# Optimization experiments

Hardware: AMD Instinct MI355X
Metric: run time of the kernel (lower is better)

The kernel has to match this reference:

```python
import jax, jax.numpy as jnp
import numpy as np

K = 50            # neighbors (self excluded)
ALPHA = 0.99      # propagation coefficient
THRESH = 0.4      # pseudo-label confidence threshold
MAXITER = 20      # CG iterations
NUM_CLASSES = 100
TOL = 1e-6        # CG relative tolerance (scipy cg tol)


def setup_inputs() -> dict:
    key = jax.random.key(0)
    k1, k2, k3 = jax.random.split(key, 3)
    N, d = 16384, 128
    X = jax.random.normal(k1, (N, d), dtype=jnp.float32)
    labels = jax.random.randint(k2, (N,), 0, NUM_CLASSES)
    labels_mask = jax.random.uniform(k3, (N,)) < 0.1
    idxs = jnp.arange(N)
    return {"X": X, "labels": labels, "labels_mask": labels_mask, "idxs": idxs}


def _label_prop(X, labels, labels_mask):
    N = X.shape[0]
    # faiss.normalize_L2 + inner-product search == cosine kNN
    Xn = X / jnp.maximum(jnp.linalg.norm(X, axis=1, keepdims=True), 1e-12)
    sims = Xn @ Xn.T                                   # [N, N]
    vals, I = jax.lax.top_k(sims, K + 1)
    Dv = vals[:, 1:] ** 3                              # drop self column, cube sims
    I = I[:, 1:]
    rows = jnp.repeat(jnp.arange(N), K)
    cols = I.reshape(-1)
    w = Dv.reshape(-1)
    # W = W + W.T with diagonal zeroed (edge-list form, never dense NxN)
    er = jnp.concatenate([rows, cols])
    ec = jnp.concatenate([cols, rows])
    ew = jnp.concatenate([w, w])
    ew = jnp.where(er == ec, 0.0, ew)
    S = jax.ops.segment_sum(ew, er, num_segments=N)
    S = jnp.where(S == 0, 1.0, S)
    Dinv = 1.0 / jnp.sqrt(S)                           # D^{-1/2}

    def A_mv(V):  # (I - alpha * D^-1/2 W D^-1/2) @ V, V: [N, C]
        U = Dinv[:, None] * V
        WU = jax.ops.segment_sum(ew[:, None] * U[ec], er, num_segments=N)
        return V - ALPHA * (Dinv[:, None] * WU)

    # per-class normalized seed vectors y (1/|labeled_c| on labeled idx of class c)
    mask_f = labels_mask.astype(jnp.float32)
    counts = jax.ops.segment_sum(mask_f, labels, num_segments=NUM_CLASSES)
    Y = (mask_f[:, None] * jax.nn.one_hot(labels, NUM_CLASSES, dtype=jnp.float32)) / jnp.maximum(counts, 1.0)[None, :]

    # batched CG (x0 = 0), all classes solved simultaneously; per-column early-stop mask
    bnorm = jnp.linalg.norm(Y, axis=0)
    x = jnp.zeros_like(Y)
    r = Y
    p = r
    rs = jnp.sum(r * r, axis=0)

    def step(carry, _):
        x, r, p, rs = carry
        active = jnp.sqrt(rs) > TOL * jnp.maximum(bnorm, 1e-30)
        Ap = A_mv(p)
        a = rs / jnp.maximum(jnp.sum(p * Ap, axis=0), 1e-30)
        a = jnp.where(active, a, 0.0)
        x = x + a * p
        r = r - a * Ap
        rs_new = jnp.sum(r * r, axis=0)
        beta = jnp.where(active, rs_new / jnp.maximum(rs, 1e-30), 0.0)
        p = jnp.where(active, r + beta * p, p)
        rs = jnp.where(active, rs_new, rs)
        return (x, r, p, rs), None

    (x, _, _, _), _ = jax.lax.scan(step, (x, r, p, rs), None, length=MAXITER)

    Z = jnp.maximum(x, 0.0)
    # torch F.normalize(Z, p=1, dim=1)
    probs_l1 = Z / jnp.maximum(jnp.sum(Z, axis=1, keepdims=True), 1e-12)
    pseudo = jax.nn.softmax(probs_l1, axis=-1)
    return pseudo


def reference(X, labels, labels_mask, idxs):
    pseudo = _label_prop(X, labels, labels_mask)
    max_probs = jnp.max(pseudo, axis=-1)
    p_labels = jnp.argmax(pseudo, axis=-1)
    masks = (max_probs >= THRESH).astype(jnp.float32)
    acc = jnp.mean((p_labels == labels).astype(jnp.float32))
    p_labels = jnp.where(labels_mask, labels, p_labels)  # overwrite labeled idx
    return p_labels, acc, masks
```

## Files before the change

kernel.cpp:

```cpp
#include <hip/hip_runtime.h>
#include <hip/hip_bf16.h>
#include <math.h>


#define N_NODES 16384
#define DIM     128
#define KNN     50
#define NCLS    100
#define PSTR    100
#define ALPHA_C 0.99f
#define TOL_C   1e-6f
#define TAU     0.20f
#define MAXITER_C 20
#define NPB     2048

__global__ __launch_bounds__(256) void k_norm(const float* __restrict__ X, float* __restrict__ Xn){
  int t = threadIdx.x;
  int row = blockIdx.x*2 + (t>>7);
  int c = t & 127;
  float v = X[(size_t)row*DIM + c];
  float s = v*v;
  #pragma unroll
  for (int o=1;o<64;o<<=1) s += __shfl_xor(s, o, 64);
  __shared__ float sw[4];
  if ((t&63)==0) sw[t>>6] = s;
  __syncthreads();
  int half = (t>>7)*2;
  float nrm = fmaxf(sqrtf(sw[half]+sw[half+1]), 1e-12f);
  Xn[(size_t)row*DIM + c] = v / nrm;
}

#define NTILE 8256
__global__ __launch_bounds__(256, 4) void k_sims(const float* __restrict__ Xn,
    int* __restrict__ cand_cnt, unsigned long long* __restrict__ cand, int CAP){
  __shared__ __align__(16) float As[32][132];
  __shared__ __align__(16) float Bs[32][132];
  const int t = threadIdx.x;
  const int tr = t >> 4, tc = t & 15;
  const int q = blockIdx.x;
  float disc = 66049.0f - 8.0f*(float)q;
  int rb = (int)((257.0f - sqrtf(disc))*0.5f);
  if (rb > 127) rb = 127;
  while (rb > 0 && rb*(257-rb)/2 > q) --rb;
  while ((rb+1)*(257-(rb+1))/2 <= q) ++rb;
  int cb = rb + (q - rb*(257-rb)/2);
  const int row0 = rb*128, col0 = cb*128;
  float acc[8][8];
  #pragma unroll
  for (int i=0;i<8;i++){
    #pragma unroll
    for (int j=0;j<8;j++) acc[i][j]=0.f;
  }
  #pragma unroll 1
  for (int h=0; h<4; ++h){
    const int koff = h*32;
    if (h) __syncthreads();
    for (int v=t; v<1024; v+=256){
      int r = v>>3, k4 = (v&7)*4;
      float4 f = *(const float4*)(Xn + (size_t)(row0+r)*DIM + koff + k4);
      As[k4+0][r]=f.x; As[k4+1][r]=f.y; As[k4+2][r]=f.z; As[k4+3][r]=f.w;
      float4 g = *(const float4*)(Xn + (size_t)(col0+r)*DIM + koff + k4);
      Bs[k4+0][r]=g.x; Bs[k4+1][r]=g.y; Bs[k4+2][r]=g.z; Bs[k4+3][r]=g.w;
    }
    __syncthreads();
    #pragma unroll 4
    for (int k=0;k<32;k++){
      float a[8], b[8];
      *(float4*)&a[0] = *(const float4*)&As[k][tr*4];
      *(float4*)&a[4] = *(const float4*)&As[k][64+tr*4];
      *(float4*)&b[0] = *(const float4*)&Bs[k][tc*4];
      *(float4*)&b[4] = *(const float4*)&Bs[k][64+tc*4];
      #pragma unroll
      for (int i=0;i<8;i++){
        #pragma unroll
        for (int j=0;j<8;j++) acc[i][j] = fmaf(a[i], b[j], acc[i][j]);
      }
    }
  }
  #pragma unroll
  for (int i=0;i<8;i++){
    int row = row0 + ((i<4) ? (tr*4+i) : (64+tr*4+i-4));
    #pragma unroll
    for (int j=0;j<8;j++){
      float v = acc[i][j];
      if (v > TAU){
        int col = col0 + ((j<4) ? (tc*4+j) : (64+tc*4+j-4));
        unsigned long long vb = (unsigned long long)__float_as_uint(v) << 32;
        if (rb == cb){
          if (col != row){
            int pos = atomicAdd(&cand_cnt[row], 1);
            if (pos < CAP) __builtin_nontemporal_store(vb | (unsigned long long)(~(unsigned int)col), &cand[(size_t)row*CAP + pos]);
          }
        } else {
          int pos = atomicAdd(&cand_cnt[row], 1);
          if (pos < CAP) __builtin_nontemporal_store(vb | (unsigned long long)(~(unsigned int)col), &cand[(size_t)row*CAP + pos]);
          int pos2 = atomicAdd(&cand_cnt[col], 1);
          if (pos2 < CAP) __builtin_nontemporal_store(vb | (unsigned long long)(~(unsigned int)row), &cand[(size_t)col*CAP + pos2]);
        }
      }
    }
  }
}

__global__ __launch_bounds__(256) void k_select(const unsigned long long* __restrict__ cand,
    const int* __restrict__ cand_cnt, int CAP,
    int* __restrict__ nbr_idx, float* __restrict__ nbr_w, int* __restrict__ flags){
  int row = blockIdx.x; int t = threadIdx.x;
  int cnt = cand_cnt[row];
  if (cnt < KNN || cnt > CAP || cnt > 1024){ if (t==0) flags[row] = 1; return; }
  __shared__ unsigned long long sk[1024];
  int N = (cnt <= 256) ? 256 : ((cnt <= 512) ? 512 : 1024);
  for (int v=t; v<N; v+=256)
    sk[v] = (v < cnt) ? cand[(size_t)row*CAP + v] : 0ull;
  __syncthreads();
  for (int k=2; k<=N; k<<=1){
    for (int j=k>>1; j>0; j>>=1){
      for (int i=t; i<N; i+=256){
        int l = i ^ j;
        if (l > i){
          unsigned long long a = sk[i], b = sk[l];
          bool desc = ((i & k) == 0);
          bool sw = desc ? (a < b) : (a > b);
          if (sw){ sk[i] = b; sk[l] = a; }
        }
      }
      __syncthreads();
    }
  }
  if (t < KNN){
    unsigned long long key = sk[t];
    float v = __uint_as_float((unsigned int)(key >> 32));
    int ii = (int)(~(unsigned int)key);
    nbr_idx[(size_t)row*KNN + t] = ii;
    nbr_w[(size_t)row*KNN + t] = v*v*v;
  }
}

__global__ __launch_bounds__(256) void k_fallback(const float* __restrict__ Xn, const int* __restrict__ flags,
    int* __restrict__ nbr_idx, float* __restrict__ nbr_w){
  int row = blockIdx.x;
  if (flags[row]==0) return;
  int t = threadIdx.x;
  __shared__ float a[DIM];
  __shared__ float cv[256]; __shared__ int ci[256];
  __shared__ float bv[KNN]; __shared__ int bi[KNN];
  __shared__ int nf; __shared__ float minv; __shared__ int mini, minpos;
  if (t < DIM) a[t] = Xn[(size_t)row*DIM + t];
  if (t==0){ nf=0; minv=1e30f; mini=-1; minpos=-1; }
  __syncthreads();
  for (int c0=0; c0<N_NODES; c0+=256){
    int col = c0 + t;
    const float* xb = Xn + (size_t)col*DIM;
    float dot = 0.f;
    for (int k=0;k<DIM;k++) dot = fmaf(a[k], xb[k], dot);
    cv[t] = (col==row) ? -1e30f : dot;
    ci[t] = col;
    __syncthreads();
    if (t==0){
      for (int u=0; u<256; u++){
        float v = cv[u]; int ix = ci[u];
        if (v <= -1e29f) continue;
        if (nf < KNN){
          bv[nf]=v; bi[nf]=ix; nf++;
          if (nf==KNN){
            minpos=0; minv=bv[0]; mini=bi[0];
            for (int q=1;q<KNN;q++) if (bv[q]<minv || (bv[q]==minv && bi[q]>mini)){minv=bv[q];mini=bi[q];minpos=q;}
          }
        } else if (v>minv || (v==minv && ix<mini)){
          bv[minpos]=v; bi[minpos]=ix;
          minpos=0; minv=bv[0]; mini=bi[0];
          for (int q=1;q<KNN;q++) if (bv[q]<minv || (bv[q]==minv && bi[q]>mini)){minv=bv[q];mini=bi[q];minpos=q;}
        }
      }
    }
    __syncthreads();
  }
  if (t==0){
    for (int aa=1; aa<KNN; aa++){
      float kv=bv[aa]; int ki=bi[aa]; int b=aa-1;
      while (b>=0 && (bv[b]<kv || (bv[b]==kv && bi[b]>ki))){ bv[b+1]=bv[b]; bi[b+1]=bi[b]; b--; }
      bv[b+1]=kv; bi[b+1]=ki;
    }
    for (int q=0;q<KNN;q++){ nbr_idx[(size_t)row*KNN+q]=bi[q]; float v=bv[q]; nbr_w[(size_t)row*KNN+q]=v*v*v; }
  }
}

__global__ void k_indeg(const int* __restrict__ nbr_idx, int* __restrict__ indeg){
  int e = blockIdx.x*blockDim.x + threadIdx.x;
  if (e < N_NODES*KNN) atomicAdd(&indeg[nbr_idx[e]], 1);
}
__global__ __launch_bounds__(256) void k_scan(const int* __restrict__ indeg, int* __restrict__ offs){
  int t = threadIdx.x;
  __shared__ int ps[256];
  int base = t*64, s = 0;
  for (int m=0;m<64;m++) s += indeg[base+m];
  ps[t] = s; __syncthreads();
  if (t==0){ int run=0; for (int i=0;i<256;i++){ int tmp=ps[i]; ps[i]=run; run+=tmp; } offs[N_NODES]=run; }
  __syncthreads();
  int run = ps[t];
  for (int m=0;m<64;m++){ offs[base+m]=run; run += indeg[base+m]; }
}
__global__ void k_fill(const int* __restrict__ nbr_idx, const float* __restrict__ nbr_w,
    const int* __restrict__ offs, int* __restrict__ fillc, int* __restrict__ rev_src, float* __restrict__ rev_w){
  int e = blockIdx.x*blockDim.x + threadIdx.x;
  if (e >= N_NODES*KNN) return;
  int i = e / KNN;
  int j = nbr_idx[e];
  int pos = offs[j] + atomicAdd(&fillc[j], 1);
  rev_src[pos] = i;
  rev_w[pos]  = nbr_w[e];
}
__global__ __launch_bounds__(256) void k_sortrev(const int* __restrict__ offs, int* __restrict__ rev_src, float* __restrict__ rev_w){
  __shared__ int   ssrc[4][512];
  __shared__ float swv [4][512];
  int w = threadIdx.x>>6, lane = threadIdx.x&63;
  int node = blockIdx.x*4 + w;
  int e0 = offs[node], e1 = offs[node+1];
  int len = e1 - e0;
  if (len <= 1 || len > 512) return;
  for (int q=lane; q<len; q+=64){ ssrc[w][q]=rev_src[e0+q]; swv[w][q]=rev_w[e0+q]; }
  if (lane==0){
    for (int a=1;a<len;a++){
      int ks=ssrc[w][a]; float kw=swv[w][a]; int b=a-1;
      while (b>=0 && ssrc[w][b]>ks){ ssrc[w][b+1]=ssrc[w][b]; swv[w][b+1]=swv[w][b]; b--; }
      ssrc[w][b+1]=ks; swv[w][b+1]=kw;
    }
  }
  for (int q=lane; q<len; q+=64){ rev_src[e0+q]=ssrc[w][q]; rev_w[e0+q]=swv[w][q]; }
}
__global__ void k_degree(const float* __restrict__ nbr_w, const int* __restrict__ offs,
    const float* __restrict__ rev_w, float* __restrict__ Dinv){
  int i = blockIdx.x*blockDim.x + threadIdx.x;
  if (i >= N_NODES) return;
  float s = 0.f;
  for (int k=0;k<KNN;k++) s += nbr_w[(size_t)i*KNN+k];
  int e0=offs[i], e1=offs[i+1];
  for (int e=e0;e<e1;e++) s += rev_w[e];
  if (s == 0.f) s = 1.f;
  Dinv[i] = 1.0f / sqrtf(s);
}
__global__ void k_normw_fwd(const int* __restrict__ nbr_idx, float* __restrict__ nbr_w, const float* __restrict__ Dinv){
  int e = blockIdx.x*blockDim.x + threadIdx.x;
  if (e >= N_NODES*KNN) return;
  int i = e / KNN; int j = nbr_idx[e];
  nbr_w[e] *= Dinv[i]*Dinv[j];
}
__global__ __launch_bounds__(256) void k_normw_rev(const int* __restrict__ offs, const int* __restrict__ rev_src,
    float* __restrict__ rev_w, const float* __restrict__ Dinv){
  int wid = (blockIdx.x*256 + threadIdx.x)>>6; int lane = threadIdx.x&63;
  if (wid >= N_NODES) return;
  float di = Dinv[wid];
  int e1 = offs[wid+1];
  for (int e=offs[wid]+lane; e<e1; e+=64) rev_w[e] *= di*Dinv[rev_src[e]];
}
__global__ __launch_bounds__(256) void k_pack(const int* __restrict__ nbr_idx, const float* __restrict__ nbr_w,
    const int* __restrict__ offs, const int* __restrict__ rev_src, const float* __restrict__ rev_w,
    int2* __restrict__ adj){
  int w = threadIdx.x>>6, lane = threadIdx.x&63;
  int node = blockIdx.x*4 + w;
  int a0 = 50*node + offs[node];
  for (int k=lane; k<KNN; k+=64)
    adj[a0+k] = make_int2(nbr_idx[(size_t)node*KNN+k], __float_as_int(nbr_w[(size_t)node*KNN+k]));
  int e0 = offs[node], e1 = offs[node+1];
  for (int e=e0+lane; e<e1; e+=64)
    adj[a0+KNN+(e-e0)] = make_int2(rev_src[e], __float_as_int(rev_w[e]));
}

__global__ void k_clscnt(const int* __restrict__ labels, const int* __restrict__ mask, int* __restrict__ cls_cnt){
  int n = blockIdx.x*blockDim.x + threadIdx.x;
  if (n < N_NODES && mask[n]) atomicAdd(&cls_cnt[labels[n]], 1);
}
__global__ void k_init(const int* __restrict__ labels, const int* __restrict__ mask, const int* __restrict__ cls_cnt,
    float* __restrict__ x, float* __restrict__ r, float* __restrict__ p){
  int idx = blockIdx.x*blockDim.x + threadIdx.x;
  if (idx >= N_NODES*PSTR) return;
  int n = idx / PSTR, c = idx - n*PSTR;
  float y = 0.f;
  if (mask[n] && labels[n]==c) y = 1.0f / fmaxf((float)cls_cnt[c], 1.0f);
  x[idx]=0.f; r[idx]=y; p[idx]=y;
}

__global__ __launch_bounds__(256) void k_spmv_pap(const float* __restrict__ p, float* __restrict__ Ap,
    const int2* __restrict__ adj, const int* __restrict__ offs,
    float* __restrict__ partT){
  int t = threadIdx.x, w = t>>6, l = t&63;
  __shared__ float sh[4][100];
  float ppx=0.f, ppy=0.f;
  if (l < 50){
    #pragma unroll
    for (int m=0;m<2;m++){
      int node = __builtin_amdgcn_readfirstlane(blockIdx.x*8 + w*2 + m);
      int a0 = 50*node + offs[node];
      int a1 = 50*(node+1) + offs[node+1];
      float accx=0.f, accy=0.f;
      for (int e=a0; e<a1; ++e){
        int2 jw = adj[e];
        float wv = __int_as_float(jw.y);
        float2 v = ((const float2*)(p + (size_t)jw.x*PSTR))[l];
        accx = fmaf(wv, v.x, accx);
        accy = fmaf(wv, v.y, accy);
      }
      size_t o = (size_t)node*PSTR;
      float2 pv = ((const float2*)(p + o))[l];
      float ax = pv.x - ALPHA_C*accx;
      float ay = pv.y - ALPHA_C*accy;
      ((float2*)(Ap + o))[l] = make_float2(ax, ay);
      ppx = fmaf(pv.x, ax, ppx);
      ppy = fmaf(pv.y, ay, ppy);
    }
    sh[w][2*l]   = ppx;
    sh[w][2*l+1] = ppy;
  }
  __syncthreads();
  if (t < 100) partT[(size_t)t*NPB + blockIdx.x] = (sh[0][t]+sh[1][t]) + (sh[2][t]+sh[3][t]);
}
__global__ __launch_bounds__(256) void k_alpha(const float* __restrict__ partT, const float* __restrict__ rs_cur,
    const float* __restrict__ bnorm, float* __restrict__ avec, int* __restrict__ actvec){
  int c = blockIdx.x, t = threadIdx.x;
  float s = 0.f;
  #pragma unroll
  for (int b=0;b<NPB/256;b++) s += partT[(size_t)c*NPB + b*256 + t];
  #pragma unroll
  for (int o=1;o<64;o<<=1) s += __shfl_xor(s, o, 64);
  __shared__ float red[4];
  if ((t&63)==0) red[t>>6] = s;
  __syncthreads();
  if (t==0){
    float tot = (red[0]+red[1]) + (red[2]+red[3]);
    float rc = rs_cur[c];
    int act = sqrtf(rc) > TOL_C*fmaxf(bnorm[c], 1e-30f);
    avec[c] = act ? rc/fmaxf(tot, 1e-30f) : 0.f;
    actvec[c] = act;
  }
}
__global__ __launch_bounds__(256) void k_update_xr(float* __restrict__ x, float* __restrict__ r,
    const float* __restrict__ p, const float* __restrict__ Ap,
    const float* __restrict__ avec, float* __restrict__ partT){
  int t = threadIdx.x, w = t>>6, l = t&63;
  __shared__ float sh[4][100];
  float rpx=0.f, rpy=0.f;
  if (l < 50){
    float2 av = ((const float2*)avec)[l];
    #pragma unroll
    for (int m=0;m<2;m++){
      int n = blockIdx.x*8 + w*2 + m;
      size_t o = (size_t)n*PSTR;
      float2 pv  = ((const float2*)(p + o))[l];
      float2 apv = ((const float2*)(Ap + o))[l];
      float2 xv  = ((const float2*)(x + o))[l];
      float2 rv  = ((const float2*)(r + o))[l];
      xv.x = fmaf(av.x, pv.x, xv.x);
      xv.y = fmaf(av.y, pv.y, xv.y);
      rv.x = rv.x - av.x*apv.x;
      rv.y = rv.y - av.y*apv.y;
      ((float2*)(x + o))[l] = xv;
      ((float2*)(r + o))[l] = rv;
      rpx = fmaf(rv.x, rv.x, rpx);
      rpy = fmaf(rv.y, rv.y, rpy);
    }
    sh[w][2*l]   = rpx;
    sh[w][2*l+1] = rpy;
  }
  __syncthreads();
  if (t < 100) partT[(size_t)t*NPB + blockIdx.x] = (sh[0][t]+sh[1][t]) + (sh[2][t]+sh[3][t]);
}
__global__ __launch_bounds__(256) void k_beta(const float* __restrict__ partT, const float* __restrict__ rs_cur,
    const int* __restrict__ actvec, float* __restrict__ rs_next, float* __restrict__ betavec){
  int c = blockIdx.x, t = threadIdx.x;
  float s = 0.f;
  #pragma unroll
  for (int b=0;b<NPB/256;b++) s += partT[(size_t)c*NPB + b*256 + t];
  #pragma unroll
  for (int o=1;o<64;o<<=1) s += __shfl_xor(s, o, 64);
  __shared__ float red[4];
  if ((t&63)==0) red[t>>6] = s;
  __syncthreads();
  if (t==0){
    float tot = (red[0]+red[1]) + (red[2]+red[3]);
    float rc = rs_cur[c];
    int act = actvec[c];
    rs_next[c] = act ? tot : rc;
    betavec[c] = act ? tot/fmaxf(rc, 1e-30f) : 0.f;
  }
}
__global__ __launch_bounds__(256) void k_update_p(float* __restrict__ p, const float* __restrict__ r,
    const int* __restrict__ actvec, const float* __restrict__ betavec){
  int t = threadIdx.x, w = t>>6, l = t&63;
  if (l >= 50) return;
  float2 bv = ((const float2*)betavec)[l];
  int2   av = ((const int2*)actvec)[l];
  #pragma unroll
  for (int m=0;m<2;m++){
    int n = blockIdx.x*8 + w*2 + m;
    size_t o = (size_t)n*PSTR;
    float2 pv = ((const float2*)(p + o))[l];
    float2 rv = ((const float2*)(r + o))[l];
    pv.x = av.x ? fmaf(bv.x, pv.x, rv.x) : pv.x;
    pv.y = av.y ? fmaf(bv.y, pv.y, rv.y) : pv.y;
    ((float2*)(p + o))[l] = pv;
  }
}
__global__ __launch_bounds__(256) void k_coldot0(const float* __restrict__ r, float* __restrict__ partT){
  int t = threadIdx.x, w = t>>6, l = t&63;
  __shared__ float sh[4][100];
  float px=0.f, py=0.f;
  if (l < 50){
    #pragma unroll
    for (int m=0;m<2;m++){
      int n = blockIdx.x*8 + w*2 + m;
      float2 rv = ((const float2*)(r + (size_t)n*PSTR))[l];
      px = fmaf(rv.x, rv.x, px);
      py = fmaf(rv.y, rv.y, py);
    }
    sh[w][2*l]   = px;
    sh[w][2*l+1] = py;
  }
  __syncthreads();
  if (t < 100) partT[(size_t)t*NPB + blockIdx.x] = (sh[0][t]+sh[1][t]) + (sh[2][t]+sh[3][t]);
}
__global__ __launch_bounds__(256) void k_rs0(const float* __restrict__ partT, float* __restrict__ rs0, float* __restrict__ bnorm){
  int c = blockIdx.x, t = threadIdx.x;
  float s = 0.f;
  #pragma unroll
  for (int b=0;b<NPB/256;b++) s += partT[(size_t)c*NPB + b*256 + t];
  #pragma unroll
  for (int o=1;o<64;o<<=1) s += __shfl_xor(s, o, 64);
  __shared__ float red[4];
  if ((t&63)==0) red[t>>6] = s;
  __syncthreads();
  if (t==0){
    float tot = (red[0]+red[1]) + (red[2]+red[3]);
    rs0[c] = tot;
    bnorm[c] = sqrtf(tot);
  }
}

__global__ __launch_bounds__(256) void k_final(const float* __restrict__ x, const int* __restrict__ labels,
    const int* __restrict__ mask, float* __restrict__ out, int* __restrict__ acc_cnt){
  int n = blockIdx.x*blockDim.x + threadIdx.x;
  if (n >= N_NODES) return;
  const float* xr = x + (size_t)n*PSTR;
  float best = xr[0]; int arg = 0;
  for (int c=1;c<NCLS;c++){ float v = xr[c]; if (v > best){ best = v; arg = c; } }
  int plab = (best > 0.f) ? arg : 0;
  if (plab == labels[n]) atomicAdd(acc_cnt, 1);
  int lab = mask[n] ? labels[n] : plab;
  out[n] = (float)lab;
  out[N_NODES + 1 + n] = 0.f;
}
__global__ void k_acc(const int* __restrict__ acc_cnt, float* __restrict__ out){
  out[N_NODES] = (float)(*acc_cnt) / (float)N_NODES;
}

extern "C" void kernel_launch(void* const* d_in, const int* in_sizes, int n_in,
                              void* d_out, int out_size, void* d_ws, size_t ws_size,
                              hipStream_t stream){
  (void)in_sizes; (void)n_in; (void)out_size;
  const float* X      = (const float*)d_in[0];
  const int*   labels = (const int*)  d_in[1];
  const int*   mask   = (const int*)  d_in[2];
  float* out = (float*)d_out;

  char* ws = (char*)d_ws;
  size_t off = 0;
  auto alloc = [&](size_t bytes)->char*{ char* pp = ws + off; off += (bytes + 255) & ~(size_t)255; return pp; };

  float* Xn      = (float*)alloc((size_t)N_NODES*DIM*4);
  int*   nbr_idx = (int*)  alloc((size_t)N_NODES*KNN*4);
  float* nbr_w   = (float*)alloc((size_t)N_NODES*KNN*4);
  int*   indeg   = (int*)  alloc((size_t)N_NODES*4);
  int*   offs    = (int*)  alloc((size_t)(N_NODES+1)*4);
  int*   fillc   = (int*)  alloc((size_t)N_NODES*4);
  int*   rev_src = (int*)  alloc((size_t)N_NODES*KNN*4);
  float* rev_w   = (float*)alloc((size_t)N_NODES*KNN*4);
  int2*  adj     = (int2*) alloc((size_t)2*N_NODES*KNN*8);
  float* Dinv    = (float*)alloc((size_t)N_NODES*4);
  int*   cls_cnt = (int*)  alloc(128*4);
  float* x  = (float*)alloc((size_t)N_NODES*PSTR*4);
  float* r  = (float*)alloc((size_t)N_NODES*PSTR*4);
  float* p  = (float*)alloc((size_t)N_NODES*PSTR*4);
  float* Ap = (float*)alloc((size_t)N_NODES*PSTR*4);
  float* rs_a   = (float*)alloc(128*4);
  float* rs_b   = (float*)alloc(128*4);
  float* avec   = (float*)alloc(128*4);
  float* betavec= (float*)alloc(128*4);
  int*   actvec = (int*)  alloc(128*4);
  float* bnorm  = (float*)alloc(128*4);
  float* partT  = (float*)alloc((size_t)100*NPB*4);
  int*   acc_cnt= (int*)  alloc(256);
  int*   flags  = (int*)  alloc((size_t)N_NODES*4);
  int*   cand_cnt=(int*)  alloc((size_t)N_NODES*4);

  size_t rem = (ws_size > off) ? (ws_size - off) : 0;
  size_t capc = rem/((size_t)N_NODES*8);
  int CAP = (int)(capc < 1024 ? capc : 1024);
  CAP &= ~7;
  unsigned long long* cand = (unsigned long long*)alloc((size_t)N_NODES*CAP*8);

  hipMemsetAsync(cand_cnt, 0, (size_t)N_NODES*4, stream);
  hipMemsetAsync(flags,    0, (size_t)N_NODES*4, stream);
  hipMemsetAsync(indeg,    0, (size_t)N_NODES*4, stream);
  hipMemsetAsync(fillc,    0, (size_t)N_NODES*4, stream);
  hipMemsetAsync(cls_cnt,  0, 128*4, stream);
  hipMemsetAsync(acc_cnt,  0, 4, stream);

  k_norm    <<<N_NODES/2, 256, 0, stream>>>(X, Xn);
  k_sims    <<<NTILE, 256, 0, stream>>>(Xn, cand_cnt, cand, CAP);
  k_select  <<<N_NODES, 256, 0, stream>>>(cand, cand_cnt, CAP, nbr_idx, nbr_w, flags);
  k_fallback<<<N_NODES, 256, 0, stream>>>(Xn, flags, nbr_idx, nbr_w);
  k_indeg   <<<3200, 256, 0, stream>>>(nbr_idx, indeg);
  k_scan    <<<1, 256, 0, stream>>>(indeg, offs);
  k_fill    <<<3200, 256, 0, stream>>>(nbr_idx, nbr_w, offs, fillc, rev_src, rev_w);
  k_sortrev <<<4096, 256, 0, stream>>>(offs, rev_src, rev_w);
  k_degree  <<<64, 256, 0, stream>>>(nbr_w, offs, rev_w, Dinv);
  k_normw_fwd<<<3200, 256, 0, stream>>>(nbr_idx, nbr_w, Dinv);
  k_normw_rev<<<4096, 256, 0, stream>>>(offs, rev_src, rev_w, Dinv);
  k_pack    <<<4096, 256, 0, stream>>>(nbr_idx, nbr_w, offs, rev_src, rev_w, adj);
  k_clscnt  <<<64, 256, 0, stream>>>(labels, mask, cls_cnt);
  k_init    <<<(N_NODES*PSTR+255)/256, 256, 0, stream>>>(labels, mask, cls_cnt, x, r, p);
  k_coldot0 <<<NPB, 256, 0, stream>>>(r, partT);
  k_rs0     <<<100, 256, 0, stream>>>(partT, rs_a, bnorm);

  for (int it=0; it<MAXITER_C; ++it){
    float* rs_cur = (it&1) ? rs_b : rs_a;
    float* rs_nxt = (it&1) ? rs_a : rs_b;
    k_spmv_pap <<<NPB, 256, 0, stream>>>(p, Ap, adj, offs, partT);
    k_alpha    <<<100, 256, 0, stream>>>(partT, rs_cur, bnorm, avec, actvec);
    k_update_xr<<<NPB, 256, 0, stream>>>(x, r, p, Ap, avec, partT);
    if (it < MAXITER_C-1){
      k_beta     <<<100, 256, 0, stream>>>(partT, rs_cur, actvec, rs_nxt, betavec);
      k_update_p <<<NPB, 256, 0, stream>>>(p, r, actvec, betavec);
    }
  }

  k_final<<<64, 256, 0, stream>>>(x, labels, mask, out, acc_cnt);
  k_acc  <<<1, 1, 0, stream>>>(acc_cnt, out);
}
```

Measured before the change: 3.045 ms.

## Sort kNN candidates per wavefront and grid-stride the fallback kernel

The candidate selection kernel now gives each 64-lane wavefront its own row and a private shared-memory buffer, four rows per block. Block-wide barriers in the bitonic sort are replaced with wave-local fences. The fallback kernel becomes a grid-stride loop over 256 blocks, so most rows that need no fallback no longer each cost a block launch. This cuts barrier and launch overhead but uses 32KB of LDS per select block. It also relies on implicit wavefront lockstep for correct shared-memory ordering in the sort.

```diff
diff --git a/kernel.cpp b/kernel.cpp
--- a/kernel.cpp
+++ b/kernel.cpp
@@ -105,17 +105,19 @@
 __global__ __launch_bounds__(256) void k_select(const unsigned long long* __restrict__ cand,
     const int* __restrict__ cand_cnt, int CAP,
     int* __restrict__ nbr_idx, float* __restrict__ nbr_w, int* __restrict__ flags){
-  int row = blockIdx.x; int t = threadIdx.x;
+  __shared__ unsigned long long skbuf[4][1024];
+  int w = threadIdx.x>>6, lane = threadIdx.x&63;
+  int row = blockIdx.x*4 + w;
   int cnt = cand_cnt[row];
-  if (cnt < KNN || cnt > CAP || cnt > 1024){ if (t==0) flags[row] = 1; return; }
-  __shared__ unsigned long long sk[1024];
+  if (cnt < KNN || cnt > CAP || cnt > 1024){ if (lane==0) flags[row] = 1; return; }
+  unsigned long long* sk = skbuf[w];
   int N = (cnt <= 256) ? 256 : ((cnt <= 512) ? 512 : 1024);
-  for (int v=t; v<N; v+=256)
+  for (int v=lane; v<N; v+=64)
     sk[v] = (v < cnt) ? cand[(size_t)row*CAP + v] : 0ull;
-  __syncthreads();
+  __threadfence_block();
   for (int k=2; k<=N; k<<=1){
     for (int j=k>>1; j>0; j>>=1){
-      for (int i=t; i<N; i+=256){
+      for (int i=lane; i<N; i+=64){
         int l = i ^ j;
         if (l > i){
           unsigned long long a = sk[i], b = sk[l];
@@ -124,27 +126,28 @@
           if (sw){ sk[i] = b; sk[l] = a; }
         }
       }
-      __syncthreads();
-    }
-  }
-  if (t < KNN){
-    unsigned long long key = sk[t];
+      __threadfence_block();
+    }
+  }
+  if (lane < KNN){
+    unsigned long long key = sk[lane];
     float v = __uint_as_float((unsigned int)(key >> 32));
     int ii = (int)(~(unsigned int)key);
-    nbr_idx[(size_t)row*KNN + t] = ii;
-    nbr_w[(size_t)row*KNN + t] = v*v*v;
+    nbr_idx[(size_t)row*KNN + lane] = ii;
+    nbr_w[(size_t)row*KNN + lane] = v*v*v;
   }
 }
 
 __global__ __launch_bounds__(256) void k_fallback(const float* __restrict__ Xn, const int* __restrict__ flags,
     int* __restrict__ nbr_idx, float* __restrict__ nbr_w){
-  int row = blockIdx.x;
-  if (flags[row]==0) return;
+  for (int row = blockIdx.x; row < N_NODES; row += gridDim.x){
+  if (flags[row]==0) continue;
   int t = threadIdx.x;
   __shared__ float a[DIM];
   __shared__ float cv[256]; __shared__ int ci[256];
   __shared__ float bv[KNN]; __shared__ int bi[KNN];
   __shared__ int nf; __shared__ float minv; __shared__ int mini, minpos;
+  __syncthreads();
   if (t < DIM) a[t] = Xn[(size_t)row*DIM + t];
   if (t==0){ nf=0; minv=1e30f; mini=-1; minpos=-1; }
   __syncthreads();
@@ -182,6 +185,8 @@
       bv[b+1]=kv; bi[b+1]=ki;
     }
     for (int q=0;q<KNN;q++){ nbr_idx[(size_t)row*KNN+q]=bi[q]; float v=bv[q]; nbr_w[(size_t)row*KNN+q]=v*v*v; }
+  }
+  __syncthreads();
   }
 }
 
@@ -506,8 +511,8 @@
 
   k_norm    <<<N_NODES/2, 256, 0, stream>>>(X, Xn);
   k_sims    <<<NTILE, 256, 0, stream>>>(Xn, cand_cnt, cand, CAP);
-  k_select  <<<N_NODES, 256, 0, stream>>>(cand, cand_cnt, CAP, nbr_idx, nbr_w, flags);
-  k_fallback<<<N_NODES, 256, 0, stream>>>(Xn, flags, nbr_idx, nbr_w);
+  k_select  <<<N_NODES/4, 256, 0, stream>>>(cand, cand_cnt, CAP, nbr_idx, nbr_w, flags);
+  k_fallback<<<256, 256, 0, stream>>>(Xn, flags, nbr_idx, nbr_w);
   k_indeg   <<<3200, 256, 0, stream>>>(nbr_idx, indeg);
   k_scan    <<<1, 256, 0, stream>>>(indeg, offs);
   k_fill    <<<3200, 256, 0, stream>>>(nbr_idx, nbr_w, offs, fillc, rev_src, rev_w);
```

Measured after the change: 3.056 ms. Within noise of the previous version (+0.4%).
